# Kernel tuning notes

Hardware: AMD Instinct MI355X
Metric: run time of the kernel (lower is better)

The kernel has to match this reference:

```python
import jax, jax.numpy as jnp
import numpy as np

B, V, K = 128, 128000, 20
_SAMPLING_EPS = 1e-5


def setup_inputs() -> dict:
    key = jax.random.key(0)
    k1, k2, k3 = jax.random.split(key, 3)
    logits = jax.random.normal(k1, (B, V), dtype=jnp.float32)
    temp = jax.random.uniform(k2, (B,), dtype=jnp.float32, minval=0.2, maxval=1.5)
    # every 4th sequence is greedy (temperature < eps)
    temp = jnp.where(jnp.arange(B) % 4 == 0, 0.0, temp)
    # uniform noise in (0,1); exponential noise is q = -log(u)
    u = jax.random.uniform(k3, (B, V), dtype=jnp.float32, minval=1e-7, maxval=1.0)
    return {"logits": logits, "temp": temp, "u": u, "max_num_logprobs": K}


def reference(logits, temp, u, max_num_logprobs):
    # apply_temperature: greedy rows (temp < eps) use temp=1.0
    t = jnp.where(temp < _SAMPLING_EPS, 1.0, temp)
    scaled = logits.astype(jnp.float32) / t[:, None]          # [B, V]
    probs = jax.nn.softmax(scaled, axis=-1)                    # [B, V]
    # greedy sample
    greedy = jnp.argmax(probs, axis=1)                         # [B]
    # random sample via exponential-race (Gumbel-max equivalent): argmax(probs / Exp(1))
    q = -jnp.log(u)                                            # Exp(1) noise
    random_sampled = jnp.argmax(probs / q, axis=1)             # [B]
    sampled = jnp.where(temp < _SAMPLING_EPS, greedy, random_sampled)
    # top-k logprobs
    logprobs = jax.nn.log_softmax(scaled, axis=-1)             # [B, V]
    topk_logprobs, topk_indices = jax.lax.top_k(logprobs, max_num_logprobs)
    return sampled, topk_logprobs, topk_indices
```

## Files before the change

### kernel.cpp

```cpp
#include <hip/hip_runtime.h>
#include <stdint.h>


#define KMAX 20
#define SAMPLING_EPS 1e-5f
#define TAU 3.0f
#define CPB 64
#define LOG2E 1.44269504f
#define SMARGIN 3e-4f

static __device__ __forceinline__ float fexp2(float x) {
#if __has_builtin(__builtin_amdgcn_exp2f)
    return __builtin_amdgcn_exp2f(x);
#else
    return exp2f(x);
#endif
}

static __device__ __forceinline__ unsigned int ord32(float v) {
    unsigned int u = __float_as_uint(v);
    return u ^ ((unsigned int)((int)u >> 31) | 0x80000000u);
}
static __device__ __forceinline__ float unord32(unsigned int x) {
    unsigned int u = (x & 0x80000000u) ? (x ^ 0x80000000u) : ~x;
    return __uint_as_float(u);
}
static __device__ __forceinline__ unsigned long long shflxor64(unsigned long long v, int off) {
    int lo = __shfl_xor((int)(unsigned int)v, off, 64);
    int hi = __shfl_xor((int)(unsigned int)(v >> 32), off, 64);
    return ((unsigned long long)(unsigned int)hi << 32) | (unsigned int)lo;
}

static __device__ __forceinline__ float gumbel_exact(float x, float inv_t, float uu, float wm) {
    const float q = (uu > 0.984375f) ? -log1pf(-wm) : -__logf(uu);
    return x * inv_t - __logf(q);
}

static __device__ __forceinline__ float gub_bound(float a, float uu) {
    return fmaf((float)__float_as_uint(1.0f - uu), -0x1p-23f, 127.0f + a);
}

__global__ __launch_bounds__(256, 4) void k1_partials(
        const float* __restrict__ logits, const float* __restrict__ u,
        const float* __restrict__ temp,
        unsigned int* __restrict__ wrec,
        unsigned int* __restrict__ cntbuf,
        uint2* __restrict__ candbuf,
        int V, int nsplit) {
    __shared__ int cnt;
    __shared__ uint2 cand[CPB];
    const int b = blockIdx.x;
    const int t = threadIdx.x;
    const int lane = t & 63;
    const int w = t >> 6;
    if (t == 0) cnt = 0;
    __syncthreads();

    const int nrows = gridDim.x / nsplit;
    const int mb = b % nrows;
    const int sp = b / nrows;
    int r = (mb * 61 + (sp >> 1)) % nrows;
    if ((nrows & (nrows - 1)) == 0) r ^= (r >> 4);
    const int slot = r * nsplit + sp;

    const float traw = temp[r];
    const bool greedy = traw < SAMPLING_EPS;
    const float inv_t = greedy ? 1.0f : (1.0f / traw);
    const float it2 = inv_t * LOG2E;

    const int nf4 = V >> 2;
    const int per = (nf4 + nsplit - 1) / nsplit;
    const int f0 = sp * per;
    const int f1 = min(f0 + per, nf4);

    const float4* __restrict__ l4 = (const float4*)(logits + (size_t)r * V);
    const float4* __restrict__ u4 = (const float4*)(u + (size_t)r * V);

    float s0 = 0.0f, s1 = 0.0f, s2 = 0.0f, s3 = 0.0f;
    float gv = -INFINITY;
    int gcol = 0;
    const float4 z4 = make_float4(0.f, 0.f, 0.f, 0.f);

#define PUSH(xv, cc) do { \
        const int pi_ = atomicAdd(&cnt, 1); \
        if (pi_ < CPB) cand[pi_] = make_uint2(__float_as_uint(xv), (unsigned)(cc)); \
    } while (0)

    if (greedy) {
        int f = f0 + t;
        bool m = (f + 256 < f1);
        float4 ca = z4, cb = z4;
        if (m) { ca = l4[f]; cb = l4[f + 256]; }
        while (m) {
            const int fn = f + 512;
            const bool mn = (fn + 256 < f1);
            float4 na = z4, nb = z4;
            if (mn) { na = l4[fn]; nb = l4[fn + 256]; }
            s0 += fexp2(ca.x * it2); s1 += fexp2(ca.y * it2);
            s2 += fexp2(ca.z * it2); s3 += fexp2(ca.w * it2);
            s0 += fexp2(cb.x * it2); s1 += fexp2(cb.y * it2);
            s2 += fexp2(cb.z * it2); s3 += fexp2(cb.w * it2);
            const float xm = fmaxf(fmaxf(fmaxf(ca.x, ca.y), fmaxf(ca.z, ca.w)),
                                   fmaxf(fmaxf(cb.x, cb.y), fmaxf(cb.z, cb.w)));
            if (xm >= TAU) {
                const int c0 = f << 2, c1 = (f + 256) << 2;
                if (ca.x >= TAU) PUSH(ca.x, c0);
                if (ca.y >= TAU) PUSH(ca.y, c0 + 1);
                if (ca.z >= TAU) PUSH(ca.z, c0 + 2);
                if (ca.w >= TAU) PUSH(ca.w, c0 + 3);
                if (cb.x >= TAU) PUSH(cb.x, c1);
                if (cb.y >= TAU) PUSH(cb.y, c1 + 1);
                if (cb.z >= TAU) PUSH(cb.z, c1 + 2);
                if (cb.w >= TAU) PUSH(cb.w, c1 + 3);
            }
            f = fn; m = mn; ca = na; cb = nb;
        }
        for (; f < f1; f += 256) {
            const float4 la = l4[f];
            s0 += fexp2(la.x * it2); s1 += fexp2(la.y * it2);
            s2 += fexp2(la.z * it2); s3 += fexp2(la.w * it2);
            const float xm = fmaxf(fmaxf(la.x, la.y), fmaxf(la.z, la.w));
            if (xm >= TAU) {
                const int c0 = f << 2;
                if (la.x >= TAU) PUSH(la.x, c0);
                if (la.y >= TAU) PUSH(la.y, c0 + 1);
                if (la.z >= TAU) PUSH(la.z, c0 + 2);
                if (la.w >= TAU) PUSH(la.w, c0 + 3);
            }
        }
    } else {
        const int fp = f0 + t;
        float4 la0 = z4, ua0 = z4;
        const bool hasp = fp < f1;
        if (hasp) { la0 = l4[fp]; ua0 = u4[fp]; }
        int f = fp + 256;
        bool m = (f + 256 < f1);
        float4 ca = z4, cb = z4, cua = z4, cub = z4;
        if (m) { ca = l4[f]; cb = l4[f + 256]; cua = u4[f]; cub = u4[f + 256]; }

        if (hasp) {
            const int c0 = fp << 2;
            s0 += fexp2(la0.x * it2); s1 += fexp2(la0.y * it2);
            s2 += fexp2(la0.z * it2); s3 += fexp2(la0.w * it2);
            { const float g = gumbel_exact(la0.x, inv_t, ua0.x, 1.0f - ua0.x);
              if (g > gv) { gv = g; gcol = c0; } }
            { const float g = gumbel_exact(la0.y, inv_t, ua0.y, 1.0f - ua0.y);
              if (g > gv) { gv = g; gcol = c0 + 1; } }
            { const float g = gumbel_exact(la0.z, inv_t, ua0.z, 1.0f - ua0.z);
              if (g > gv) { gv = g; gcol = c0 + 2; } }
            { const float g = gumbel_exact(la0.w, inv_t, ua0.w, 1.0f - ua0.w);
              if (g > gv) { gv = g; gcol = c0 + 3; } }
            const float xm = fmaxf(fmaxf(la0.x, la0.y), fmaxf(la0.z, la0.w));
            if (xm >= TAU) {
                if (la0.x >= TAU) PUSH(la0.x, c0);
                if (la0.y >= TAU) PUSH(la0.y, c0 + 1);
                if (la0.z >= TAU) PUSH(la0.z, c0 + 2);
                if (la0.w >= TAU) PUSH(la0.w, c0 + 3);
            }
        }
        float gmax = gv;
        #pragma unroll
        for (int off = 1; off < 64; off <<= 1) gmax = fmaxf(gmax, __shfl_xor(gmax, off, 64));
        float gvs2 = fmaf(gmax, LOG2E, -SMARGIN);

#define EX(gj, xv, uu, cc) \
        if ((gj) > gvs2) { \
            const float wm_ = 1.0f - (uu); \
            const float ge_ = gumbel_exact(xv, inv_t, uu, wm_); \
            if (ge_ > gv) { gv = ge_; gcol = (cc); gvs2 = fmaf(ge_, LOG2E, -SMARGIN); } \
        }

        while (m) {
            const int fn = f + 512;
            const bool mn = (fn + 256 < f1);
            float4 na = z4, nb = z4, nua = z4, nub = z4;
            if (mn) { na = l4[fn]; nb = l4[fn + 256]; nua = u4[fn]; nub = u4[fn + 256]; }

            const float a0 = ca.x * it2, a1 = ca.y * it2, a2 = ca.z * it2, a3 = ca.w * it2;
            const float a4 = cb.x * it2, a5 = cb.y * it2, a6 = cb.z * it2, a7 = cb.w * it2;
            s0 += fexp2(a0); s1 += fexp2(a1); s2 += fexp2(a2); s3 += fexp2(a3);
            s0 += fexp2(a4); s1 += fexp2(a5); s2 += fexp2(a6); s3 += fexp2(a7);
            const float g0 = gub_bound(a0, cua.x), g1 = gub_bound(a1, cua.y);
            const float g2 = gub_bound(a2, cua.z), g3 = gub_bound(a3, cua.w);
            const float g4 = gub_bound(a4, cub.x), g5 = gub_bound(a5, cub.y);
            const float g6 = gub_bound(a6, cub.z), g7 = gub_bound(a7, cub.w);
            const float gm = fmaxf(fmaxf(fmaxf(g0, g1), fmaxf(g2, g3)),
                                   fmaxf(fmaxf(g4, g5), fmaxf(g6, g7)));
            if (gm > gvs2) {
                const int c0 = f << 2, c1 = (f + 256) << 2;
                EX(g0, ca.x, cua.x, c0)
                EX(g1, ca.y, cua.y, c0 + 1)
                EX(g2, ca.z, cua.z, c0 + 2)
                EX(g3, ca.w, cua.w, c0 + 3)
                EX(g4, cb.x, cub.x, c1)
                EX(g5, cb.y, cub.y, c1 + 1)
                EX(g6, cb.z, cub.z, c1 + 2)
                EX(g7, cb.w, cub.w, c1 + 3)
            }
            const float xm = fmaxf(fmaxf(fmaxf(ca.x, ca.y), fmaxf(ca.z, ca.w)),
                                   fmaxf(fmaxf(cb.x, cb.y), fmaxf(cb.z, cb.w)));
            if (xm >= TAU) {
                const int c0 = f << 2, c1 = (f + 256) << 2;
                if (ca.x >= TAU) PUSH(ca.x, c0);
                if (ca.y >= TAU) PUSH(ca.y, c0 + 1);
                if (ca.z >= TAU) PUSH(ca.z, c0 + 2);
                if (ca.w >= TAU) PUSH(ca.w, c0 + 3);
                if (cb.x >= TAU) PUSH(cb.x, c1);
                if (cb.y >= TAU) PUSH(cb.y, c1 + 1);
                if (cb.z >= TAU) PUSH(cb.z, c1 + 2);
                if (cb.w >= TAU) PUSH(cb.w, c1 + 3);
            }
            f = fn; m = mn;
            ca = na; cb = nb; cua = nua; cub = nub;
        }
        for (; f < f1; f += 256) {
            const float4 la = l4[f];
            const float4 ua = u4[f];
            const float a0 = la.x * it2, a1 = la.y * it2, a2 = la.z * it2, a3 = la.w * it2;
            s0 += fexp2(a0); s1 += fexp2(a1); s2 += fexp2(a2); s3 += fexp2(a3);
            const float g0 = gub_bound(a0, ua.x), g1 = gub_bound(a1, ua.y);
            const float g2 = gub_bound(a2, ua.z), g3 = gub_bound(a3, ua.w);
            const float gm = fmaxf(fmaxf(g0, g1), fmaxf(g2, g3));
            if (gm > gvs2) {
                const int c0 = f << 2;
                EX(g0, la.x, ua.x, c0)
                EX(g1, la.y, ua.y, c0 + 1)
                EX(g2, la.z, ua.z, c0 + 2)
                EX(g3, la.w, ua.w, c0 + 3)
            }
            const float xm = fmaxf(fmaxf(la.x, la.y), fmaxf(la.z, la.w));
            if (xm >= TAU) {
                const int c0 = f << 2;
                if (la.x >= TAU) PUSH(la.x, c0);
                if (la.y >= TAU) PUSH(la.y, c0 + 1);
                if (la.z >= TAU) PUSH(la.z, c0 + 2);
                if (la.w >= TAU) PUSH(la.w, c0 + 3);
            }
        }
#undef EX
    }
#undef PUSH

    float s = (s0 + s1) + (s2 + s3);
    #pragma unroll
    for (int off = 1; off < 64; off <<= 1) s += __shfl_xor(s, off, 64);
    unsigned long long gk = greedy ? 0ull
        : (((unsigned long long)ord32(gv) << 32) | (unsigned int)~(unsigned int)gcol);
    #pragma unroll
    for (int off = 1; off < 64; off <<= 1) {
        const unsigned long long o = shflxor64(gk, off);
        gk = (o > gk) ? o : gk;
    }
    if (lane == 0) {
        unsigned int* rp = wrec + (size_t)(slot * 4 + w) * 4;
        rp[0] = __float_as_uint(s);
        rp[1] = __float_as_uint(unord32((unsigned int)(gk >> 32)));
        rp[2] = ~(unsigned int)gk;
    }
    __syncthreads();
    const int c = cnt;
    if (t == 0) cntbuf[slot] = (unsigned)c;
    if (t < min(c, CPB)) candbuf[(size_t)slot * CPB + t] = cand[t];
}

__global__ __launch_bounds__(64) void k2_finalize(
        const unsigned int* __restrict__ wrec, const unsigned int* __restrict__ cntbuf,
        const uint2* __restrict__ candbuf, const float* __restrict__ logits,
        const float* __restrict__ temp, float* __restrict__ out,
        int B, int V, int K, int nsplit) {
    __shared__ unsigned long long kbuf[512];
    const int r = blockIdx.x;
    const int lane = threadIdx.x;
    const int NW = nsplit * 4;

    const float traw = temp[r];
    const bool greedy = traw < SAMPLING_EPS;
    const float tt = greedy ? 1.0f : traw;

    float s = 0.0f;
    unsigned long long gk = 0ull;
    if (lane < NW) {
        const unsigned int* rp = wrec + (size_t)(r * NW + lane) * 4;
        s = __uint_as_float(rp[0]);
        gk = ((unsigned long long)ord32(__uint_as_float(rp[1])) << 32) | (unsigned int)~rp[2];
    }
    #pragma unroll
    for (int off = 1; off < 64; off <<= 1) s += __shfl_xor(s, off, 64);
    #pragma unroll
    for (int off = 1; off < 64; off <<= 1) {
        const unsigned long long o = shflxor64(gk, off);
        gk = (o > gk) ? o : gk;
    }
    const float lS = logf(s);

    const int cnt_raw = (lane < nsplit) ? (int)cntbuf[r * nsplit + lane] : 0;
    const int cntc = min(cnt_raw, CPB);
    const bool ovf = __ballot(cnt_raw > CPB) != 0ull;
    int incl = cntc;
    #pragma unroll
    for (int d = 1; d < 64; d <<= 1) {
        const int o = __shfl_up(incl, d, 64);
        if (lane >= d) incl += o;
    }
    const int T = __shfl(incl, 63, 64);
    const int off0 = incl - cntc;

    unsigned long long keys[8];
    #pragma unroll
    for (int jj = 0; jj < 8; ++jj) keys[jj] = 0ull;

    if (!ovf && T >= K && T <= 512) {
        if (lane < nsplit) {
            const uint2* cb = candbuf + (size_t)(r * nsplit + lane) * CPB;
            for (int i = 0; i < cntc; ++i) {
                const uint2 e = cb[i];
                kbuf[off0 + i] = ((unsigned long long)ord32(__uint_as_float(e.x)) << 32)
                               | (unsigned int)~e.y;
            }
        }
        __syncthreads();
        #pragma unroll
        for (int jj = 0; jj < 8; ++jj) {
            const int idx = lane + 64 * jj;
            if (idx < T) keys[jj] = kbuf[idx];
        }
    } else {
        unsigned long long mykey = ((unsigned long long)0x007FFFFFu) << 32;
        unsigned long long minkey = mykey;
        float vmin = -INFINITY;
        const float* lr = logits + (size_t)r * V;
        for (int base = 0; base < V; base += 64) {
            const int i = base + lane;
            const float x = (i < V) ? lr[i] : -INFINITY;
            unsigned long long cm = __ballot((i < V) && (x >= vmin));
            while (cm) {
                const int src = (int)__builtin_ctzll(cm);
                cm &= cm - 1;
                const float cv = __shfl(x, src, 64);
                const int cc = __shfl(i, src, 64);
                const unsigned long long ck =
                    ((unsigned long long)ord32(cv) << 32) | (unsigned int)~(unsigned int)cc;
                if (ck > minkey) {
                    const bool own = (lane < K) && (mykey == minkey);
                    const unsigned long long om = __ballot(own);
                    if (lane == (int)__builtin_ctzll(om)) mykey = ck;
                    unsigned long long mk = (lane < K) ? mykey : ~0ull;
                    #pragma unroll
                    for (int o2 = 1; o2 < 64; o2 <<= 1) {
                        const unsigned long long o = shflxor64(mk, o2);
                        mk = (o < mk) ? o : mk;
                    }
                    minkey = mk;
                    vmin = unord32((unsigned int)(mk >> 32));
                }
            }
        }
        keys[0] = (lane < K) ? mykey : 0ull;
    }

    float* out_s  = out;
    float* out_lp = out + B;
    float* out_ix = out + B + (size_t)B * K;

    unsigned int top1 = 0;
    for (int k = 0; k < K; ++k) {
        unsigned long long loc = keys[0];
        #pragma unroll
        for (int jj = 1; jj < 8; ++jj) loc = (keys[jj] > loc) ? keys[jj] : loc;
        #pragma unroll
        for (int off = 1; off < 64; off <<= 1) {
            const unsigned long long o = shflxor64(loc, off);
            loc = (o > loc) ? o : loc;
        }
        #pragma unroll
        for (int jj = 0; jj < 8; ++jj) if (keys[jj] == loc) keys[jj] = 0ull;
        if (lane == 0) {
            const unsigned int col = ~(unsigned int)loc;
            const float v = unord32((unsigned int)(loc >> 32));
            out_lp[(size_t)r * K + k] = v / tt - lS;
            out_ix[(size_t)r * K + k] = (float)col;
            if (k == 0) top1 = col;
        }
    }
    if (lane == 0) {
        out_s[r] = (float)(greedy ? top1 : (~(unsigned int)gk));
    }
}

extern "C" void kernel_launch(void* const* d_in, const int* in_sizes, int n_in,
                              void* d_out, int out_size, void* d_ws, size_t ws_size,
                              hipStream_t stream) {
    const float* logits = (const float*)d_in[0];
    const float* temp   = (const float*)d_in[1];
    const float* u      = (const float*)d_in[2];
    const int B = in_sizes[1];
    const int V = in_sizes[0] / B;
    int K = (out_size - B) / (2 * B);
    if (K > KMAX) K = KMAX;
    if (K < 1) K = 1;

    int nsplit = 16;
    while (nsplit > 1 && (size_t)B * nsplit * 580 > ws_size) nsplit >>= 1;
    const int blocks = B * nsplit;

    unsigned int* wrec   = (unsigned int*)d_ws;
    unsigned int* cntbuf = wrec + (size_t)blocks * 16;
    uint2*        candbf = (uint2*)(cntbuf + blocks);

    k1_partials<<<dim3(blocks), dim3(256), 0, stream>>>(
        logits, u, temp, wrec, cntbuf, candbf, V, nsplit);
    k2_finalize<<<dim3(B), dim3(64), 0, stream>>>(
        wrec, cntbuf, candbf, logits, temp, (float*)d_out, B, V, K, nsplit);
}
```

Measured before the change: 163.7 us.

## Fuse finalize into partials kernel via last-block-per-row atomic counter

Merges the second finalize kernel into the first. Each block bumps a per-row atomic counter, and the last block of each row (wave 0 only) runs the reduction, candidate merge and top-k output. This removes a kernel launch and its inter-kernel gap. In exchange it adds a hipMemsetAsync to clear the counters, threadfences, and relaxed atomic loads. The finalize tail now runs at the end of whichever block finishes last, which may leave a serial tail.

```diff
diff --git a/kernel.cpp b/kernel.cpp
--- a/kernel.cpp
+++ b/kernel.cpp
@@ -30,6 +30,12 @@
     int hi = __shfl_xor((int)(unsigned int)(v >> 32), off, 64);
     return ((unsigned long long)(unsigned int)hi << 32) | (unsigned int)lo;
 }
+static __device__ __forceinline__ unsigned int aload_u32(const unsigned int* p) {
+    return __hip_atomic_load(p, __ATOMIC_RELAXED, __HIP_MEMORY_SCOPE_AGENT);
+}
+static __device__ __forceinline__ unsigned long long aload_u64(const unsigned long long* p) {
+    return __hip_atomic_load(p, __ATOMIC_RELAXED, __HIP_MEMORY_SCOPE_AGENT);
+}
 
 static __device__ __forceinline__ float gumbel_exact(float x, float inv_t, float uu, float wm) {
     const float q = (uu > 0.984375f) ? -log1pf(-wm) : -__logf(uu);
@@ -40,15 +46,19 @@
     return fmaf((float)__float_as_uint(1.0f - uu), -0x1p-23f, 127.0f + a);
 }
 
-__global__ __launch_bounds__(256, 4) void k1_partials(
+__global__ __launch_bounds__(256, 4) void k1_fused(
         const float* __restrict__ logits, const float* __restrict__ u,
         const float* __restrict__ temp,
-        unsigned int* __restrict__ wrec,
-        unsigned int* __restrict__ cntbuf,
-        uint2* __restrict__ candbuf,
-        int V, int nsplit) {
+        unsigned int* wrec,
+        unsigned int* cntbuf,
+        uint2* candbuf,
+        unsigned int* rowcnt,
+        float* __restrict__ out,
+        int B, int V, int K, int nsplit) {
     __shared__ int cnt;
     __shared__ uint2 cand[CPB];
+    __shared__ unsigned long long kbuf[512];
+    __shared__ int lastflag;
     const int b = blockIdx.x;
     const int t = threadIdx.x;
     const int lane = t & 63;
@@ -261,39 +271,40 @@
     const int c = cnt;
     if (t == 0) cntbuf[slot] = (unsigned)c;
     if (t < min(c, CPB)) candbuf[(size_t)slot * CPB + t] = cand[t];
-}
-
-__global__ __launch_bounds__(64) void k2_finalize(
-        const unsigned int* __restrict__ wrec, const unsigned int* __restrict__ cntbuf,
-        const uint2* __restrict__ candbuf, const float* __restrict__ logits,
-        const float* __restrict__ temp, float* __restrict__ out,
-        int B, int V, int K, int nsplit) {
-    __shared__ unsigned long long kbuf[512];
-    const int r = blockIdx.x;
-    const int lane = threadIdx.x;
+
+    __threadfence();
+    __syncthreads();
+    if (t == 0) {
+        const unsigned int old = atomicAdd(&rowcnt[r], 1u);
+        lastflag = (old == (unsigned)(nsplit - 1)) ? 1 : 0;
+    }
+    __syncthreads();
+    if (!lastflag || w != 0) return;
+    __threadfence();
+
     const int NW = nsplit * 4;
-
-    const float traw = temp[r];
-    const bool greedy = traw < SAMPLING_EPS;
     const float tt = greedy ? 1.0f : traw;
 
-    float s = 0.0f;
-    unsigned long long gk = 0ull;
+    float fs = 0.0f;
+    unsigned long long fgk = 0ull;
     if (lane < NW) {
         const unsigned int* rp = wrec + (size_t)(r * NW + lane) * 4;
-        s = __uint_as_float(rp[0]);
-        gk = ((unsigned long long)ord32(__uint_as_float(rp[1])) << 32) | (unsigned int)~rp[2];
-    }
-    #pragma unroll
-    for (int off = 1; off < 64; off <<= 1) s += __shfl_xor(s, off, 64);
+        const unsigned int a0 = aload_u32(rp + 0);
+        const unsigned int a1 = aload_u32(rp + 1);
+        const unsigned int a2 = aload_u32(rp + 2);
+        fs = __uint_as_float(a0);
+        fgk = ((unsigned long long)ord32(__uint_as_float(a1)) << 32) | (unsigned int)~a2;
+    }
+    #pragma unroll
+    for (int off = 1; off < 64; off <<= 1) fs += __shfl_xor(fs, off, 64);
     #pragma unroll
     for (int off = 1; off < 64; off <<= 1) {
-        const unsigned long long o = shflxor64(gk, off);
-        gk = (o > gk) ? o : gk;
-    }
-    const float lS = logf(s);
-
-    const int cnt_raw = (lane < nsplit) ? (int)cntbuf[r * nsplit + lane] : 0;
+        const unsigned long long o = shflxor64(fgk, off);
+        fgk = (o > fgk) ? o : fgk;
+    }
+    const float lS = logf(fs);
+
+    const int cnt_raw = (lane < nsplit) ? (int)aload_u32(&cntbuf[r * nsplit + lane]) : 0;
     const int cntc = min(cnt_raw, CPB);
     const bool ovf = __ballot(cnt_raw > CPB) != 0ull;
     int incl = cntc;
@@ -311,14 +322,17 @@
 
     if (!ovf && T >= K && T <= 512) {
         if (lane < nsplit) {
-            const uint2* cb = candbuf + (size_t)(r * nsplit + lane) * CPB;
+            const unsigned long long* cb =
+                (const unsigned long long*)(candbuf + (size_t)(r * nsplit + lane) * CPB);
             for (int i = 0; i < cntc; ++i) {
-                const uint2 e = cb[i];
-                kbuf[off0 + i] = ((unsigned long long)ord32(__uint_as_float(e.x)) << 32)
-                               | (unsigned int)~e.y;
-            }
-        }
-        __syncthreads();
+                const unsigned long long e = aload_u64(cb + i);
+                const unsigned int vbits = (unsigned int)e;
+                const unsigned int col   = (unsigned int)(e >> 32);
+                kbuf[off0 + i] = ((unsigned long long)ord32(__uint_as_float(vbits)) << 32)
+                               | (unsigned int)~col;
+            }
+        }
+        __threadfence_block();
         #pragma unroll
         for (int jj = 0; jj < 8; ++jj) {
             const int idx = lane + 64 * jj;
@@ -383,7 +397,7 @@
         }
     }
     if (lane == 0) {
-        out_s[r] = (float)(greedy ? top1 : (~(unsigned int)gk));
+        out_s[r] = (float)(greedy ? top1 : (~(unsigned int)fgk));
     }
 }
 
@@ -400,15 +414,16 @@
     if (K < 1) K = 1;
 
     int nsplit = 16;
-    while (nsplit > 1 && (size_t)B * nsplit * 580 > ws_size) nsplit >>= 1;
+    while (nsplit > 1 && ((size_t)B * nsplit * 580 + (size_t)B * 4) > ws_size) nsplit >>= 1;
     const int blocks = B * nsplit;
 
     unsigned int* wrec   = (unsigned int*)d_ws;
     unsigned int* cntbuf = wrec + (size_t)blocks * 16;
     uint2*        candbf = (uint2*)(cntbuf + blocks);
-
-    k1_partials<<<dim3(blocks), dim3(256), 0, stream>>>(
-        logits, u, temp, wrec, cntbuf, candbf, V, nsplit);
-    k2_finalize<<<dim3(B), dim3(64), 0, stream>>>(
-        wrec, cntbuf, candbf, logits, temp, (float*)d_out, B, V, K, nsplit);
-}
+    unsigned int* rowcnt = (unsigned int*)(candbf + (size_t)blocks * CPB);
+
+    hipMemsetAsync((void*)rowcnt, 0, (size_t)B * sizeof(unsigned int), stream);
+
+    k1_fused<<<dim3(blocks), dim3(256), 0, stream>>>(
+        logits, u, temp, wrec, cntbuf, candbf, rowcnt, (float*)d_out, B, V, K, nsplit);
+}
```

Result: slower. 378.9 us (+131.5%).
